# Kernel optimization log

Measured on AMD Instinct MI355X. Metric: run time of the kernel, lower is better.

Reference implementation:

```python
import jax, jax.numpy as jnp
import numpy as np

H = 16          # num_attention_heads
DH = 64         # attention_head_size = hidden // heads
WINDOW = 128    # window_size
GLOBAL_RATIO = 0.1
SCALE = 1.0 / np.sqrt(DH)


def _combined_mask(seq_len):
    # sliding window: |i-j| <= window_size // 2
    pos = jnp.arange(seq_len)
    dist = pos[None, :] - pos[:, None]
    window_mask = jnp.abs(dist) <= (WINDOW // 2)
    # global tokens: first max(1, int(S * ratio)) positions, full row+col
    num_global = max(1, int(seq_len * GLOBAL_RATIO))
    is_global = pos < num_global
    global_mask = is_global[:, None] | is_global[None, :]
    return window_mask | global_mask  # [S, S] bool


def setup_inputs() -> dict:
    key = jax.random.key(0)
    ks = jax.random.split(key, 9)
    B, S, Dm = 2, 2048, 1024
    s = 0.02
    return {
        "hidden_states": jax.random.normal(ks[0], (B, S, Dm), jnp.float32),
        "Wq": jax.random.normal(ks[1], (Dm, Dm), jnp.float32) * s,
        "bq": jax.random.normal(ks[2], (Dm,), jnp.float32) * s,
        "Wk": jax.random.normal(ks[3], (Dm, Dm), jnp.float32) * s,
        "bk": jax.random.normal(ks[4], (Dm,), jnp.float32) * s,
        "Wv": jax.random.normal(ks[5], (Dm, Dm), jnp.float32) * s,
        "bv": jax.random.normal(ks[6], (Dm,), jnp.float32) * s,
        "Wo": jax.random.normal(ks[7], (Dm, Dm), jnp.float32) * s,
        "bo": jax.random.normal(ks[8], (Dm,), jnp.float32) * s,
    }


def reference(hidden_states, Wq, bq, Wk, bk, Wv, bv, Wo, bo):
    B, S, Dm = hidden_states.shape

    def heads(x):  # [B,S,Dm] -> [B,H,S,Dh]
        return x.reshape(B, S, H, DH).transpose(0, 2, 1, 3)

    q = heads(hidden_states @ Wq.T + bq)
    k = heads(hidden_states @ Wk.T + bk)
    v = heads(hidden_states @ Wv.T + bv)

    scores = jnp.einsum("bhqd,bhkd->bhqk", q, k) * SCALE
    mask = _combined_mask(S)  # [S,S] bool, True = attend
    scores = scores + jnp.where(mask, 0.0, -10000.0)[None, None]

    probs = jax.nn.softmax(scores, axis=-1)
    ctx = jnp.einsum("bhqk,bhkd->bhqd", probs, v)
    ctx = ctx.transpose(0, 2, 1, 3).reshape(B, S, Dm)
    return ctx @ Wo.T + bo
```

## Files before the change

kernel.cpp:

```cpp
#include <hip/hip_runtime.h>


#define B_   2
#define S_   2048
#define DM   1024
#define H_   16
#define NG   204
#define BS_  4096
#define SCL2 0.1803368801111204f
#define NEGF -3.0e38f

typedef unsigned short u16;
typedef unsigned int   u32;
typedef __attribute__((ext_vector_type(8))) short frag8;
typedef __attribute__((ext_vector_type(4))) float f32x4;

#define MFMA16(A, Bf, C) __builtin_amdgcn_mfma_f32_16x16x32_bf16((A), (Bf), (C), 0, 0, 0)
#define GLD16(g, l)                                                              \
  __builtin_amdgcn_global_load_lds((const __attribute__((address_space(1))) u32*)(g), \
                                   (__attribute__((address_space(3))) u32*)(l), 16, 0, 0)
#define EXP2(x) exp2f(x)

__device__ __forceinline__ u16 f2bf(float f) {
  union { float f; u32 u; } c; c.f = f;
  u32 u = c.u + 0x7fffu + ((c.u >> 16) & 1u);
  return (u16)(u >> 16);
}

__global__ void cvt_all(const float* __restrict__ X,  const float* __restrict__ Wq,
                        const float* __restrict__ Wk, const float* __restrict__ Wv,
                        const float* __restrict__ Wo,
                        u16* Xb, u16* Wqb, u16* Wkb, u16* Wvb, u16* Wob) {
  const int chunk = blockIdx.y;
  const float* src; u16* dst;
  if (chunk < 4)      { src = X + (size_t)chunk * 1048576; dst = Xb + (size_t)chunk * 1048576; }
  else if (chunk == 4){ src = Wq; dst = Wqb; }
  else if (chunk == 5){ src = Wk; dst = Wkb; }
  else if (chunk == 6){ src = Wv; dst = Wvb; }
  else                { src = Wo; dst = Wob; }
  int i = blockIdx.x * 256 + threadIdx.x;
  float4 v = ((const float4*)src)[i];
  u32 lo = (u32)f2bf(v.x) | ((u32)f2bf(v.y) << 16);
  u32 hi = (u32)f2bf(v.z) | ((u32)f2bf(v.w) << 16);
  ((uint2*)dst)[i] = make_uint2(lo, hi);
}

__device__ __forceinline__ void gemm_mainloop(const u16* __restrict__ A, const u16* __restrict__ Bm,
                                              int bm, int bn, u16* As, u16* Bs,
                                              f32x4 acc[4][4]) {
  const int tid = threadIdx.x;
  const int wv = tid >> 6, lane = tid & 63, l15 = lane & 15, quad = lane >> 4;
  const int wm = wv & 1, wn = wv >> 1;

  const u16* gA[4]; const u16* gB[4];
#pragma unroll
  for (int c = 0; c < 4; ++c) {
    int idx = (wv * 4 + c) * 64 + lane;
    int r = idx >> 3;
    int cb = (idx & 7) ^ (r & 7);
    gA[c] = A  + (size_t)(bm + r) * DM + cb * 8;
    gB[c] = Bm + (size_t)(bn + r) * DM + cb * 8;
  }

  int offA[4][2], offB[4][2];
#pragma unroll
  for (int i = 0; i < 4; ++i)
#pragma unroll
    for (int h = 0; h < 2; ++h) {
      int mA = wm * 64 + i * 16 + l15;
      int mB = wn * 64 + i * 16 + l15;
      int cb = (quad + h * 4) ^ (l15 & 7);
      offA[i][h] = ((mA << 3) + cb) << 4;
      offB[i][h] = ((mB << 3) + cb) << 4;
    }

  for (int k0 = 0; k0 < DM; k0 += 64) {
#pragma unroll
    for (int c = 0; c < 4; ++c) {
      GLD16(gA[c] + k0, (char*)As + (wv * 4 + c) * 1024);
      GLD16(gB[c] + k0, (char*)Bs + (wv * 4 + c) * 1024);
    }
    __syncthreads();
    frag8 af[4][2], bf[4][2];
#pragma unroll
    for (int i = 0; i < 4; ++i) {
      af[i][0] = *(const frag8*)((const char*)As + offA[i][0]);
      af[i][1] = *(const frag8*)((const char*)As + offA[i][1]);
      bf[i][0] = *(const frag8*)((const char*)Bs + offB[i][0]);
      bf[i][1] = *(const frag8*)((const char*)Bs + offB[i][1]);
    }
#pragma unroll
    for (int h = 0; h < 2; ++h)
#pragma unroll
      for (int i = 0; i < 4; ++i)
#pragma unroll
        for (int j = 0; j < 4; ++j)
          acc[i][j] = MFMA16(af[i][h], bf[j][h], acc[i][j]);
    __syncthreads();
  }
}

__global__ __launch_bounds__(256, 3) void gemm_qkv(const u16* __restrict__ Xb,
    const u16* __restrict__ Wqb, const u16* __restrict__ Wkb, const u16* __restrict__ Wvb,
    const float* __restrict__ bq, const float* __restrict__ bk, const float* __restrict__ bv,
    u16* __restrict__ Qb, u16* __restrict__ Kb, u16* __restrict__ Vt) {
  __shared__ u16 As[8192], Bs[8192];
  const int bm = blockIdx.y * 128;
  const int which = blockIdx.x >> 3;
  const int bnl = (blockIdx.x & 7) * 128;
  const u16* W = (which == 0) ? Wqb : (which == 1) ? Wkb : Wvb;
  const float* bias = (which == 0) ? bq : (which == 1) ? bk : bv;

  f32x4 acc[4][4] = {};
  gemm_mainloop(Xb, W, bm, bnl, As, Bs, acc);

  const int tid = threadIdx.x, wv = tid >> 6, lane = tid & 63, l15 = lane & 15, quad = lane >> 4;
  const int wm = wv & 1, wn = wv >> 1;
  if (which < 2) {
    u16* O = (which == 0) ? Qb : Kb;
#pragma unroll
    for (int j = 0; j < 4; ++j) {
      int col = bnl + wn * 64 + j * 16 + l15;
      float bb = bias[col];
#pragma unroll
      for (int i = 0; i < 4; ++i) {
        int row0 = bm + wm * 64 + i * 16 + quad * 4;
#pragma unroll
        for (int r = 0; r < 4; ++r)
          O[(size_t)(row0 + r) * DM + col] = f2bf(acc[i][j][r] + bb);
      }
    }
  } else {
#pragma unroll
    for (int j = 0; j < 4; ++j) {
      int col = bnl + wn * 64 + j * 16 + l15;
      float bb = bias[col];
#pragma unroll
      for (int i = 0; i < 4; ++i) {
        int row0 = bm + wm * 64 + i * 16 + quad * 4;
        u32 lo = (u32)f2bf(acc[i][j][0] + bb) | ((u32)f2bf(acc[i][j][1] + bb) << 16);
        u32 hi = (u32)f2bf(acc[i][j][2] + bb) | ((u32)f2bf(acc[i][j][3] + bb) << 16);
        *(uint2*)&Vt[(size_t)col * BS_ + row0] = make_uint2(lo, hi);
      }
    }
  }
}

__global__ __launch_bounds__(256, 3) void gemm_wo(const u16* __restrict__ Cx,
    const u16* __restrict__ Wob, const float* __restrict__ bo, float* __restrict__ out) {
  __shared__ u16 As[4096], Bs[8192];
  const int tid = threadIdx.x;
  const int wv = tid >> 6, lane = tid & 63, l15 = lane & 15, quad = lane >> 4;
  const int bm = blockIdx.y * 64, bn = blockIdx.x * 128;

  const u16* gA[2]; const u16* gB[4];
  int ldsA[2], ldsB[4];
#pragma unroll
  for (int c = 0; c < 2; ++c) {
    int slot = c * 256 + wv * 64 + lane;
    int r = slot >> 3, cb = (slot & 7) ^ (r & 7);
    gA[c] = Cx + (size_t)(bm + r) * DM + cb * 8;
    ldsA[c] = (c * 256 + wv * 64) * 16;
  }
#pragma unroll
  for (int c = 0; c < 4; ++c) {
    int slot = c * 256 + wv * 64 + lane;
    int r = slot >> 3, cb = (slot & 7) ^ (r & 7);
    gB[c] = Wob + (size_t)(bn + r) * DM + cb * 8;
    ldsB[c] = (c * 256 + wv * 64) * 16;
  }

  int offA[2], offB[8][2];
#pragma unroll
  for (int h = 0; h < 2; ++h) {
    int rowA = wv * 16 + l15;
    offA[h] = ((rowA << 3) + ((quad + h * 4) ^ (l15 & 7))) << 4;
#pragma unroll
    for (int j = 0; j < 8; ++j) {
      int rowB = j * 16 + l15;
      offB[j][h] = ((rowB << 3) + ((quad + h * 4) ^ (l15 & 7))) << 4;
    }
  }

  f32x4 acc[8] = {};
  for (int k0 = 0; k0 < DM; k0 += 64) {
#pragma unroll
    for (int c = 0; c < 2; ++c) GLD16(gA[c] + k0, (char*)As + ldsA[c]);
#pragma unroll
    for (int c = 0; c < 4; ++c) GLD16(gB[c] + k0, (char*)Bs + ldsB[c]);
    __syncthreads();
    frag8 af0 = *(const frag8*)((const char*)As + offA[0]);
    frag8 af1 = *(const frag8*)((const char*)As + offA[1]);
#pragma unroll
    for (int j = 0; j < 8; ++j) {
      frag8 bf0 = *(const frag8*)((const char*)Bs + offB[j][0]);
      frag8 bf1 = *(const frag8*)((const char*)Bs + offB[j][1]);
      acc[j] = MFMA16(af0, bf0, acc[j]);
      acc[j] = MFMA16(af1, bf1, acc[j]);
    }
    __syncthreads();
  }

#pragma unroll
  for (int j = 0; j < 8; ++j) {
    int col = bn + j * 16 + l15;
    float bb = bo[col];
    int row0 = bm + wv * 16 + quad * 4;
#pragma unroll
    for (int r = 0; r < 4; ++r)
      out[(size_t)(row0 + r) * DM + col] = acc[j][r] + bb;
  }
}

__global__ __launch_bounds__(256) void attn_kernel(const u16* __restrict__ Q,
                                                   const u16* __restrict__ K,
                                                   const u16* __restrict__ Vt,
                                                   u16* __restrict__ Ctx) {
  __shared__ u16 Ks[2][4096];
  __shared__ u16 Vs[2][4096];
  __shared__ u16 Ps[4][16 * 76];

  const int tid = threadIdx.x, w = tid >> 6, lane = tid & 63, l15 = lane & 15, quad = lane >> 4;
  const int blk = blockIdx.x;
  const int xcd = blk & 7, slot = blk >> 3;
  const int bh = xcd + 8 * (slot & 3);
  const int strip = slot >> 2;
  const int b = bh >> 4, h = bh & 15;
  const int q0 = strip * 64;
  const int qw = q0 + w * 16;

  const u16* qrow = Q + (size_t)(b * S_ + qw + l15) * DM + h * 64;
  frag8 aq0 = *(const frag8*)(qrow + quad * 8);
  frag8 aq1 = *(const frag8*)(qrow + quad * 8 + 32);

  const u16* gK[2]; const u16* gV[2]; int ldso[2];
#pragma unroll
  for (int c = 0; c < 2; ++c) {
    int sl = (w * 2 + c) * 64 + lane;
    int r = sl >> 3, cb = (sl & 7) ^ (r & 7);
    gK[c] = K  + (size_t)(b * S_ + r) * DM + h * 64 + cb * 8;
    gV[c] = Vt + (size_t)(h * 64 + r) * BS_ + (size_t)b * S_ + cb * 8;
    ldso[c] = (w * 2 + c) * 1024;
  }

  int offF[4][2];
#pragma unroll
  for (int g = 0; g < 4; ++g)
#pragma unroll
    for (int hh = 0; hh < 2; ++hh)
      offF[g][hh] = (((g * 16 + l15) << 3) + ((quad + hh * 4) ^ (l15 & 7))) << 4;

  int qidx[4]; bool qglob[4];
#pragma unroll
  for (int r = 0; r < 4; ++r) { qidx[r] = qw + quad * 4 + r; qglob[r] = qidx[r] < NG; }

  f32x4 o[4] = {};
  float lsum[4] = {0.f, 0.f, 0.f, 0.f};

  auto activef = [&](int t) {
    int k0 = t * 64;
    return (q0 < NG) || (k0 < NG) || (k0 + 63 >= q0 - 64 && k0 <= q0 + 127);
  };
  auto nextt = [&](int cur) { int n = cur + 1; while (n < 32 && !activef(n)) ++n; return n; };
  auto stage = [&](int t, int buf) {
#pragma unroll
    for (int c = 0; c < 2; ++c) {
      GLD16(gK[c] + (size_t)t * 64 * DM, (char*)Ks[buf] + ldso[c]);
      GLD16(gV[c] + t * 64,              (char*)Vs[buf] + ldso[c]);
    }
  };

  int kt = 0, p = 0;
  stage(0, 0);
  for (;;) {
    int ktn = nextt(kt);
    bool more = ktn < 32;
    __syncthreads();
    if (more) stage(ktn, p ^ 1);

    const char* kb_ = (const char*)Ks[p];
    const char* vb_ = (const char*)Vs[p];

    f32x4 sc[4] = {};
#pragma unroll
    for (int kg = 0; kg < 4; ++kg) {
      frag8 bk0 = *(const frag8*)(kb_ + offF[kg][0]);
      frag8 bk1 = *(const frag8*)(kb_ + offF[kg][1]);
      sc[kg] = MFMA16(aq0, bk0, sc[kg]);
      sc[kg] = MFMA16(aq1, bk1, sc[kg]);
    }
    frag8 bvf[4][2];
#pragma unroll
    for (int nt = 0; nt < 4; ++nt) {
      bvf[nt][0] = *(const frag8*)(vb_ + offF[nt][0]);
      bvf[nt][1] = *(const frag8*)(vb_ + offF[nt][1]);
    }

    const int k0 = kt * 64;
    const bool domask = (strip > 2) && (kt > 2);
    float pr[4][4];
    if (domask) {
#pragma unroll
      for (int kg = 0; kg < 4; ++kg) {
        int kc = k0 + kg * 16 + l15;
        bool kglob = kc < NG;
#pragma unroll
        for (int r = 0; r < 4; ++r) {
          int d = qidx[r] - kc;
          bool act = ((unsigned)(d + 64) <= 128u) || qglob[r] || kglob;
          float pv = EXP2(act ? sc[kg][r] * SCL2 : NEGF);
          pr[kg][r] = pv; lsum[r] += pv;
        }
      }
    } else {
#pragma unroll
      for (int kg = 0; kg < 4; ++kg)
#pragma unroll
        for (int r = 0; r < 4; ++r) {
          float pv = EXP2(sc[kg][r] * SCL2);
          pr[kg][r] = pv; lsum[r] += pv;
        }
    }

#pragma unroll
    for (int kg = 0; kg < 4; ++kg)
#pragma unroll
      for (int r = 0; r < 4; ++r)
        Ps[w][(quad * 4 + r) * 76 + kg * 16 + l15] = f2bf(pr[kg][r]);
    __asm__ volatile("s_waitcnt lgkmcnt(0)" ::: "memory");
    frag8 ap0 = *(const frag8*)&Ps[w][l15 * 76 + quad * 8];
    frag8 ap1 = *(const frag8*)&Ps[w][l15 * 76 + quad * 8 + 32];

#pragma unroll
    for (int nt = 0; nt < 4; ++nt) {
      o[nt] = MFMA16(ap0, bvf[nt][0], o[nt]);
      o[nt] = MFMA16(ap1, bvf[nt][1], o[nt]);
    }

    if (!more) break;
    kt = ktn; p ^= 1;
  }

#pragma unroll
  for (int off = 8; off; off >>= 1)
#pragma unroll
    for (int r = 0; r < 4; ++r) lsum[r] += __shfl_xor(lsum[r], off);

#pragma unroll
  for (int r = 0; r < 4; ++r) {
    float inv = 1.0f / lsum[r];
    int row = qw + quad * 4 + r;
    u16* crow = Ctx + (size_t)((size_t)b * S_ + row) * DM + h * 64;
#pragma unroll
    for (int nt = 0; nt < 4; ++nt)
      crow[nt * 16 + l15] = f2bf(o[nt][r] * inv);
  }
}

extern "C" void kernel_launch(void* const* d_in, const int* in_sizes, int n_in,
                              void* d_out, int out_size, void* d_ws, size_t ws_size,
                              hipStream_t stream) {
  const float* X  = (const float*)d_in[0];
  const float* Wq = (const float*)d_in[1];
  const float* bq = (const float*)d_in[2];
  const float* Wk = (const float*)d_in[3];
  const float* bk = (const float*)d_in[4];
  const float* Wv = (const float*)d_in[5];
  const float* bv = (const float*)d_in[6];
  const float* Wo = (const float*)d_in[7];
  const float* bo = (const float*)d_in[8];
  float* out = (float*)d_out;

  u16* ws = (u16*)d_ws;
  const size_t NX = (size_t)BS_ * DM;
  const size_t NW = (size_t)DM * DM;
  u16* Xb  = ws;
  u16* Wqb = Xb + NX;
  u16* Wkb = Wqb + NW;
  u16* Wvb = Wkb + NW;
  u16* Wob = Wvb + NW;
  u16* Qb  = Wob + NW;
  u16* Kb  = Qb + NX;
  u16* Vt  = Kb + NX;
  u16* Cx  = Vt + NX;

  cvt_all<<<dim3(1024, 8), 256, 0, stream>>>(X, Wq, Wk, Wv, Wo, Xb, Wqb, Wkb, Wvb, Wob);
  gemm_qkv<<<dim3(24, 32), 256, 0, stream>>>(Xb, Wqb, Wkb, Wvb, bq, bk, bv, Qb, Kb, Vt);
  attn_kernel<<<1024, 256, 0, stream>>>(Qb, Kb, Vt, Cx);
  gemm_wo<<<dim3(8, 64), 256, 0, stream>>>(Cx, Wob, bo, out);
}
```

Measured before the change: 185.1 us.

## Compute transposed scores so probabilities feed PV MFMA directly from registers

```diff
diff --git a/kernel.cpp b/kernel.cpp
--- a/kernel.cpp
+++ b/kernel.cpp
@@ -13,9 +13,20 @@
 typedef unsigned short u16;
 typedef unsigned int   u32;
 typedef __attribute__((ext_vector_type(8))) short frag8;
+typedef __attribute__((ext_vector_type(4))) short frag4;
 typedef __attribute__((ext_vector_type(4))) float f32x4;
 
 #define MFMA16(A, Bf, C) __builtin_amdgcn_mfma_f32_16x16x32_bf16((A), (Bf), (C), 0, 0, 0)
+
+__device__ __forceinline__ f32x4 mfma_16x16x16_bf16(frag4 a, frag4 b, f32x4 c) {
+#if defined(__HIP_DEVICE_COMPILE__)
+  return __builtin_amdgcn_mfma_f32_16x16x16bf16_1k(a, b, c, 0, 0, 0);
+#else
+  (void)a; (void)b;
+  return c;
+#endif
+}
+
 #define GLD16(g, l)                                                              \
   __builtin_amdgcn_global_load_lds((const __attribute__((address_space(1))) u32*)(g), \
                                    (__attribute__((address_space(3))) u32*)(l), 16, 0, 0)
@@ -25,6 +36,10 @@
   union { float f; u32 u; } c; c.f = f;
   u32 u = c.u + 0x7fffu + ((c.u >> 16) & 1u);
   return (u16)(u >> 16);
+}
+__device__ __forceinline__ u16 f2bfc(float f) {
+  union { float f; u32 u; } c; c.f = f;
+  return (u16)((c.u + 0x8000u) >> 16);
 }
 
 __global__ void cvt_all(const float* __restrict__ X,  const float* __restrict__ Wq,
@@ -212,13 +227,12 @@
   }
 }
 
-__global__ __launch_bounds__(256) void attn_kernel(const u16* __restrict__ Q,
-                                                   const u16* __restrict__ K,
-                                                   const u16* __restrict__ Vt,
-                                                   u16* __restrict__ Ctx) {
+__global__ __launch_bounds__(256, 4) void attn_kernel(const u16* __restrict__ Q,
+                                                      const u16* __restrict__ K,
+                                                      const u16* __restrict__ Vt,
+                                                      u16* __restrict__ Ctx) {
   __shared__ u16 Ks[2][4096];
   __shared__ u16 Vs[2][4096];
-  __shared__ u16 Ps[4][16 * 76];
 
   const int tid = threadIdx.x, w = tid >> 6, lane = tid & 63, l15 = lane & 15, quad = lane >> 4;
   const int blk = blockIdx.x;
@@ -230,8 +244,8 @@
   const int qw = q0 + w * 16;
 
   const u16* qrow = Q + (size_t)(b * S_ + qw + l15) * DM + h * 64;
-  frag8 aq0 = *(const frag8*)(qrow + quad * 8);
-  frag8 aq1 = *(const frag8*)(qrow + quad * 8 + 32);
+  frag8 bq0 = *(const frag8*)(qrow + quad * 8);
+  frag8 bq1 = *(const frag8*)(qrow + quad * 8 + 32);
 
   const u16* gK[2]; const u16* gV[2]; int ldso[2];
 #pragma unroll
@@ -243,19 +257,21 @@
     ldso[c] = (w * 2 + c) * 1024;
   }
 
-  int offF[4][2];
-#pragma unroll
-  for (int g = 0; g < 4; ++g)
-#pragma unroll
-    for (int hh = 0; hh < 2; ++hh)
-      offF[g][hh] = (((g * 16 + l15) << 3) + ((quad + hh * 4) ^ (l15 & 7))) << 4;
-
-  int qidx[4]; bool qglob[4];
-#pragma unroll
-  for (int r = 0; r < 4; ++r) { qidx[r] = qw + quad * 4 + r; qglob[r] = qidx[r] < NG; }
+  int offKb[2];
+#pragma unroll
+  for (int hh = 0; hh < 2; ++hh)
+    offKb[hh] = ((l15 << 3) + ((quad + hh * 4) ^ (l15 & 7))) << 4;
+  int offVb[4];
+#pragma unroll
+  for (int kg = 0; kg < 4; ++kg)
+    offVb[kg] = ((((l15 << 3) + (((kg << 1) | (quad >> 1)) ^ (l15 & 7))) << 4)
+                 | ((quad & 1) << 3));
+
+  const int qidx = qw + l15;
+  const bool qglob = qidx < NG;
 
   f32x4 o[4] = {};
-  float lsum[4] = {0.f, 0.f, 0.f, 0.f};
+  float lsum = 0.f;
 
   auto activef = [&](int t) {
     int k0 = t * 64;
@@ -281,79 +297,69 @@
     const char* kb_ = (const char*)Ks[p];
     const char* vb_ = (const char*)Vs[p];
 
-    f32x4 sc[4] = {};
+    f32x4 st[4] = {};
 #pragma unroll
     for (int kg = 0; kg < 4; ++kg) {
-      frag8 bk0 = *(const frag8*)(kb_ + offF[kg][0]);
-      frag8 bk1 = *(const frag8*)(kb_ + offF[kg][1]);
-      sc[kg] = MFMA16(aq0, bk0, sc[kg]);
-      sc[kg] = MFMA16(aq1, bk1, sc[kg]);
-    }
-    frag8 bvf[4][2];
-#pragma unroll
-    for (int nt = 0; nt < 4; ++nt) {
-      bvf[nt][0] = *(const frag8*)(vb_ + offF[nt][0]);
-      bvf[nt][1] = *(const frag8*)(vb_ + offF[nt][1]);
+      frag8 ak0 = *(const frag8*)(kb_ + offKb[0] + kg * 2048);
+      frag8 ak1 = *(const frag8*)(kb_ + offKb[1] + kg * 2048);
+      st[kg] = MFMA16(ak0, bq0, st[kg]);
+      st[kg] = MFMA16(ak1, bq1, st[kg]);
     }
 
     const int k0 = kt * 64;
     const bool domask = (strip > 2) && (kt > 2);
-    float pr[4][4];
+    frag4 pk[4];
     if (domask) {
 #pragma unroll
       for (int kg = 0; kg < 4; ++kg) {
-        int kc = k0 + kg * 16 + l15;
-        bool kglob = kc < NG;
+        float pr[4];
 #pragma unroll
         for (int r = 0; r < 4; ++r) {
-          int d = qidx[r] - kc;
-          bool act = ((unsigned)(d + 64) <= 128u) || qglob[r] || kglob;
-          float pv = EXP2(act ? sc[kg][r] * SCL2 : NEGF);
-          pr[kg][r] = pv; lsum[r] += pv;
+          int kc = k0 + kg * 16 + quad * 4 + r;
+          int d = qidx - kc;
+          bool act = ((unsigned)(d + 64) <= 128u) || qglob || (kc < NG);
+          float pv = EXP2(act ? st[kg][r] * SCL2 : NEGF);
+          pr[r] = pv; lsum += pv;
         }
+        pk[kg] = frag4{(short)f2bfc(pr[0]), (short)f2bfc(pr[1]),
+                       (short)f2bfc(pr[2]), (short)f2bfc(pr[3])};
       }
     } else {
 #pragma unroll
-      for (int kg = 0; kg < 4; ++kg)
+      for (int kg = 0; kg < 4; ++kg) {
+        float pr[4];
 #pragma unroll
         for (int r = 0; r < 4; ++r) {
-          float pv = EXP2(sc[kg][r] * SCL2);
-          pr[kg][r] = pv; lsum[r] += pv;
+          float pv = EXP2(st[kg][r] * SCL2);
+          pr[r] = pv; lsum += pv;
         }
-    }
-
-#pragma unroll
-    for (int kg = 0; kg < 4; ++kg)
-#pragma unroll
-      for (int r = 0; r < 4; ++r)
-        Ps[w][(quad * 4 + r) * 76 + kg * 16 + l15] = f2bf(pr[kg][r]);
-    __asm__ volatile("s_waitcnt lgkmcnt(0)" ::: "memory");
-    frag8 ap0 = *(const frag8*)&Ps[w][l15 * 76 + quad * 8];
-    frag8 ap1 = *(const frag8*)&Ps[w][l15 * 76 + quad * 8 + 32];
-
-#pragma unroll
-    for (int nt = 0; nt < 4; ++nt) {
-      o[nt] = MFMA16(ap0, bvf[nt][0], o[nt]);
-      o[nt] = MFMA16(ap1, bvf[nt][1], o[nt]);
-    }
+        pk[kg] = frag4{(short)f2bfc(pr[0]), (short)f2bfc(pr[1]),
+                       (short)f2bfc(pr[2]), (short)f2bfc(pr[3])};
+      }
+    }
+
+#pragma unroll
+    for (int nt = 0; nt < 4; ++nt)
+#pragma unroll
+      for (int kg = 0; kg < 4; ++kg) {
+        frag4 av = *(const frag4*)(vb_ + offVb[kg] + nt * 2048);
+        o[nt] = mfma_16x16x16_bf16(av, pk[kg], o[nt]);
+      }
 
     if (!more) break;
     kt = ktn; p ^= 1;
   }
 
-#pragma unroll
-  for (int off = 8; off; off >>= 1)
-#pragma unroll
-    for (int r = 0; r < 4; ++r) lsum[r] += __shfl_xor(lsum[r], off);
-
-#pragma unroll
-  for (int r = 0; r < 4; ++r) {
-    float inv = 1.0f / lsum[r];
-    int row = qw + quad * 4 + r;
-    u16* crow = Ctx + (size_t)((size_t)b * S_ + row) * DM + h * 64;
-#pragma unroll
-    for (int nt = 0; nt < 4; ++nt)
-      crow[nt * 16 + l15] = f2bf(o[nt][r] * inv);
+  lsum += __shfl_xor(lsum, 16);
+  lsum += __shfl_xor(lsum, 32);
+  float inv = 1.0f / lsum;
+
+  u16* crow = Ctx + (size_t)((size_t)b * S_ + qw + l15) * DM + h * 64;
+#pragma unroll
+  for (int nt = 0; nt < 4; ++nt) {
+    u32 lo = (u32)f2bf(o[nt][0] * inv) | ((u32)f2bf(o[nt][1] * inv) << 16);
+    u32 hi = (u32)f2bf(o[nt][2] * inv) | ((u32)f2bf(o[nt][3] * inv) << 16);
+    *(uint2*)&crow[nt * 16 + quad * 4] = make_uint2(lo, hi);
   }
 }
 
```

Result: faster. 179.9 us (-2.8%).
